# Kernel optimization log

Hardware: AMD Instinct MI355X
Metric: run time of the kernel (lower is better)

## Reference

```python
import jax, jax.numpy as jnp
import numpy as np

B, IN = 8192, 8000
C, S, O = 16, 500, 64          # num_chunks, chunk_size, fc_repr_dim
F = C * O                       # fc_0_out_feat = 1024
E, D, T = 8, 512, 2            # num_experts, fc_task_dim, num_tasks
NC = (32, 2)                    # num_classes per task
EPS = 1e-5


def _bn(h, g, b, axis):
    # training-mode BatchNorm1d: biased variance over the batch axis
    m = h.mean(axis=axis, keepdims=True)
    v = h.var(axis=axis, keepdims=True)
    return (h - m) * jax.lax.rsqrt(v + EPS) * g + b


def _swish(x):
    return x * jax.nn.sigmoid(x)


def setup_inputs() -> dict:
    key = jax.random.key(0)
    ks = jax.random.split(key, 10)
    s = 0.02
    return {
        "x": jax.random.normal(ks[0], (B, IN), dtype=jnp.float32),
        "w0": jax.random.normal(ks[1], (C, O, S), dtype=jnp.float32) * s,
        "b0": jnp.zeros((F,), jnp.float32),
        "bn0_g": jnp.ones((F,), jnp.float32),
        "bn0_b": jnp.zeros((F,), jnp.float32),
        "gate_w": jax.random.normal(ks[2], (T, F, E), dtype=jnp.float32) * s,
        "gate_b": jnp.zeros((T, E), jnp.float32),
        "exp_w": jax.random.normal(ks[3], (E, F, D), dtype=jnp.float32) * s,
        "exp_bn_g": jnp.ones((E, D), jnp.float32),
        "exp_bn_b": jnp.zeros((E, D), jnp.float32),
        "task_w": jax.random.normal(ks[4], (T, D, D), dtype=jnp.float32) * s,
        "task_bn_g": jnp.ones((T, D), jnp.float32),
        "task_bn_b": jnp.zeros((T, D), jnp.float32),
        "fin_w_a": jax.random.normal(ks[5], (D, NC[0]), dtype=jnp.float32) * s,
        "fin_b_a": jnp.zeros((NC[0],), jnp.float32),
        "fin_w_b": jax.random.normal(ks[6], (D, NC[1]), dtype=jnp.float32) * s,
        "fin_b_b": jnp.zeros((NC[1],), jnp.float32),
    }


def reference(x, w0, b0, bn0_g, bn0_b, gate_w, gate_b, exp_w, exp_bn_g,
              exp_bn_b, task_w, task_bn_g, task_bn_b, fin_w_a, fin_b_a,
              fin_w_b, fin_b_b):
    b = x.shape[0]
    # SplitLinear: block-diagonal linear over C chunks of size S -> O each
    h0 = jnp.einsum('bcs,cos->bco', x.reshape(b, C, S), w0).reshape(b, F) + b0
    h0 = _swish(_bn(h0, bn0_g, bn0_b, axis=0))                  # [B, F]
    # per-task gates with softmax over experts
    gates = jax.nn.softmax(
        jnp.einsum('bf,tfe->tbe', h0, gate_w) + gate_b[:, None, :], axis=-1)
    # expert branches: Linear(no bias) + BN + Swish, vectorized over experts
    eh = jnp.einsum('bf,efd->bed', h0, exp_w)                   # [B, E, D]
    eh = _swish(_bn(eh, exp_bn_g, exp_bn_b, axis=0))
    # gate-weighted sum over experts, per task
    mix = jnp.einsum('tbe,bed->tbd', gates, eh)                 # [T, B, D]
    # task branches: Linear(no bias) + BN + Swish
    th = jnp.einsum('tbd,tdk->tbk', mix, task_w)
    th = _swish(_bn(th, task_bn_g[:, None, :], task_bn_b[:, None, :], axis=1))
    out_a = th[0] @ fin_w_a + fin_b_a                           # [B, 32]
    out_b = th[1] @ fin_w_b + fin_b_b                           # [B, 2]
    return jnp.concatenate([out_a, out_b], axis=1)             # [B, 34]
```

## Files before the change

kernel.cpp:

```cpp
#include <hip/hip_runtime.h>
#include <math.h>

#define B_ 8192
#define IN_ 8000
#define C_ 16
#define S_ 500
#define O_ 64
#define F_ 1024
#define E_ 8
#define D_ 512
#define T_ 2
#define OUTW 34
#define EPS_ 1e-5f

typedef __attribute__((ext_vector_type(8))) short bf16x8;
typedef __attribute__((ext_vector_type(4))) float f32x4;

__device__ __forceinline__ float swishf(float x) {
    return x / (1.0f + __expf(-x));
}

__device__ __forceinline__ unsigned short f2bf(float f) {
    union { float f; unsigned u; } c;
    c.f = f;
    unsigned r = c.u + 0x7fffu + ((c.u >> 16) & 1u);
    return (unsigned short)(r >> 16);
}
__device__ __forceinline__ float bf2f(unsigned short b) {
    union { unsigned u; float f; } c;
    c.u = ((unsigned)b) << 16;
    return c.f;
}

__device__ __forceinline__ void gld16(const void* g, void* l) {
    __builtin_amdgcn_global_load_lds(
        (const __attribute__((address_space(1))) void*)g,
        (__attribute__((address_space(3))) void*)l, 16, 0, 0);
}

__global__ __launch_bounds__(256) void k_split(const float* __restrict__ x,
                                               const float* __restrict__ w0,
                                               const float* __restrict__ b0,
                                               unsigned short* __restrict__ h0raw,
                                               float* __restrict__ psum,
                                               float* __restrict__ psq) {
    __shared__ __align__(16) unsigned short As[128 * 72];
    __shared__ __align__(16) unsigned short Bs[64 * 72];
    int tid = threadIdx.x;
    int c = blockIdx.y;
    int brow0 = blockIdx.x * 128;
    const float* xp = x + (size_t)brow0 * IN_ + c * S_;
    const float* wp = w0 + (size_t)c * O_ * S_;

    int w = tid >> 6, lane = tid & 63;
    int l15 = lane & 15, quad = lane >> 4;
    int wm = w * 32;

    f32x4 acc[2][4] = {};

    for (int k0 = 0; k0 < 512; k0 += 64) {
#pragma unroll
        for (int i = 0; i < 8; i++) {
            int li = tid + i * 256;
            int row = li >> 4, c4 = li & 15;
            int gk = k0 + c4 * 4;
            float4 v = make_float4(0.f, 0.f, 0.f, 0.f);
            if (gk + 3 < S_) v = *(const float4*)(xp + (size_t)row * IN_ + gk);
            unsigned short u[4] = { f2bf(v.x), f2bf(v.y), f2bf(v.z), f2bf(v.w) };
            *(ushort4*)&As[row * 72 + c4 * 4] = *(ushort4*)u;
        }
#pragma unroll
        for (int i = 0; i < 4; i++) {
            int li = tid + i * 256;
            int row = li >> 4, c4 = li & 15;
            int gk = k0 + c4 * 4;
            float4 v = make_float4(0.f, 0.f, 0.f, 0.f);
            if (gk + 3 < S_) v = *(const float4*)(wp + (size_t)row * S_ + gk);
            unsigned short u[4] = { f2bf(v.x), f2bf(v.y), f2bf(v.z), f2bf(v.w) };
            *(ushort4*)&Bs[row * 72 + c4 * 4] = *(ushort4*)u;
        }
        __syncthreads();
#pragma unroll
        for (int kk = 0; kk < 64; kk += 32) {
            bf16x8 af[2], wf[4];
#pragma unroll
            for (int i = 0; i < 2; i++)
                af[i] = *(const bf16x8*)&As[(wm + i * 16 + l15) * 72 + kk + quad * 8];
#pragma unroll
            for (int j = 0; j < 4; j++)
                wf[j] = *(const bf16x8*)&Bs[(j * 16 + l15) * 72 + kk + quad * 8];
#pragma unroll
            for (int i = 0; i < 2; i++)
#pragma unroll
                for (int j = 0; j < 4; j++)
                    acc[i][j] = __builtin_amdgcn_mfma_f32_16x16x32_bf16(af[i], wf[j], acc[i][j], 0, 0, 0);
        }
        __syncthreads();
    }

    int colbase = c * O_;
    float sj[4], qj[4];
#pragma unroll
    for (int j = 0; j < 4; j++) {
        int col = j * 16 + l15;
        float bb = b0[colbase + col];
        float s = 0.f, q = 0.f;
#pragma unroll
        for (int i = 0; i < 2; i++) {
#pragma unroll
            for (int reg = 0; reg < 4; reg++) {
                float v = acc[i][j][reg] + bb;
                int rl = wm + i * 16 + quad * 4 + reg;
                h0raw[(size_t)(brow0 + rl) * F_ + colbase + col] = f2bf(v);
                s += v; q += v * v;
            }
        }
        s += __shfl_down(s, 32, 64); s += __shfl_down(s, 16, 64);
        q += __shfl_down(q, 32, 64); q += __shfl_down(q, 16, 64);
        sj[j] = s; qj[j] = q;
    }
    __syncthreads();
    float* red = (float*)As;
    if (lane < 16) {
#pragma unroll
        for (int j = 0; j < 4; j++) {
            int col = j * 16 + l15;
            red[col * 4 + w] = sj[j];
            red[256 + col * 4 + w] = qj[j];
        }
    }
    __syncthreads();
    if (tid < 64) {
        float ss = red[tid * 4] + red[tid * 4 + 1] + red[tid * 4 + 2] + red[tid * 4 + 3];
        float qq = red[256 + tid * 4] + red[256 + tid * 4 + 1] + red[256 + tid * 4 + 2] + red[256 + tid * 4 + 3];
        size_t idx = (size_t)blockIdx.x * F_ + colbase + tid;
        psum[idx] = ss; psq[idx] = qq;
    }
}

__global__ __launch_bounds__(64) void k_stats_b(const float* __restrict__ psum,
                                                const float* __restrict__ psq,
                                                int N, int YS,
                                                const float* __restrict__ g,
                                                const float* __restrict__ beta,
                                                unsigned long long gslab,
                                                float* __restrict__ scale,
                                                float* __restrict__ shift,
                                                unsigned long long oslab) {
    int n = blockIdx.x * 64 + threadIdx.x;
    int z = blockIdx.z;
    float s = 0.f, q = 0.f;
    for (int y = 0; y < YS; y++) {
        size_t idx = ((size_t)(z * YS + y)) * N + n;
        s += psum[idx]; q += psq[idx];
    }
    float mean = s * (1.0f / B_);
    float var = q * (1.0f / B_) - mean * mean;
    float sc = g[z * gslab + n] * rsqrtf(var + EPS_);
    scale[z * oslab + n] = sc;
    shift[z * oslab + n] = beta[z * gslab + n] - mean * sc;
}

__global__ __launch_bounds__(256) void k_wt(const float* __restrict__ in,
                                            unsigned short* __restrict__ out,
                                            int K, int N) {
    __shared__ float t[32][33];
    int k0 = blockIdx.x * 32, n0 = blockIdx.y * 32, z = blockIdx.z;
    const float* ip = in + (size_t)z * K * N;
    unsigned short* op = out + (size_t)z * N * K;
    int tn = threadIdx.x & 31, tk = threadIdx.x >> 5;
#pragma unroll
    for (int p = 0; p < 4; p++) {
        int k = tk + p * 8;
        t[k][tn] = ip[(size_t)(k0 + k) * N + n0 + tn];
    }
    __syncthreads();
    int tk2 = threadIdx.x & 31, tn2 = threadIdx.x >> 5;
#pragma unroll
    for (int p = 0; p < 4; p++) {
        int n = tn2 + p * 8;
        op[(size_t)(n0 + n) * K + k0 + tk2] = f2bf(t[tk2][n]);
    }
}

__global__ __launch_bounds__(256) void k_bnswish(const unsigned short* __restrict__ h0,
                                                 const float* __restrict__ scale,
                                                 const float* __restrict__ shift,
                                                 unsigned short* __restrict__ h0bf) {
    int tid = threadIdx.x;
    int f0 = tid * 4;
    float4 sc4 = *(const float4*)(scale + f0);
    float4 sh4 = *(const float4*)(shift + f0);
    float scv[4] = { sc4.x, sc4.y, sc4.z, sc4.w };
    float shv[4] = { sh4.x, sh4.y, sh4.z, sh4.w };
    size_t base = (size_t)blockIdx.x * 4 * F_ + f0;
#pragma unroll
    for (int r = 0; r < 4; r++) {
        ushort4 u = *(const ushort4*)(h0 + base + (size_t)r * F_);
        unsigned short uu[4] = { u.x, u.y, u.z, u.w };
        unsigned short ov[4];
#pragma unroll
        for (int j = 0; j < 4; j++)
            ov[j] = f2bf(swishf(scv[j] * bf2f(uu[j]) + shv[j]));
        *(ushort4*)(h0bf + base + (size_t)r * F_) = *(ushort4*)ov;
    }
}

__global__ __launch_bounds__(256) void k_gates(const unsigned short* __restrict__ h0bf,
                                               const float* __restrict__ gate_w,
                                               const float* __restrict__ gate_b,
                                               float* __restrict__ gates) {
    __shared__ __align__(16) unsigned short gwt[16 * 1032];
    int tid = threadIdx.x;
    for (int idx = tid; idx < 16 * 1024; idx += 256) {
        int col = idx >> 10, f = idx & 1023;
        int t = col >> 3, e = col & 7;
        gwt[col * 1032 + f] = f2bf(gate_w[(size_t)t * (F_ * E_) + (size_t)f * E_ + e]);
    }
    __syncthreads();
    int w = tid >> 6, lane = tid & 63;
    int l15 = lane & 15, quad = lane >> 4;
    int r0 = blockIdx.x * 128 + w * 32;
    f32x4 acc[2] = {};
    const unsigned short* a0p = h0bf + (size_t)(r0 + l15) * F_ + quad * 8;
    const unsigned short* a1p = a0p + (size_t)16 * F_;
    const unsigned short* wp = &gwt[l15 * 1032 + quad * 8];
#pragma unroll 4
    for (int k0 = 0; k0 < F_; k0 += 32) {
        bf16x8 wf  = *(const bf16x8*)(wp + k0);
        bf16x8 af0 = *(const bf16x8*)(a0p + k0);
        bf16x8 af1 = *(const bf16x8*)(a1p + k0);
        acc[0] = __builtin_amdgcn_mfma_f32_16x16x32_bf16(af0, wf, acc[0], 0, 0, 0);
        acc[1] = __builtin_amdgcn_mfma_f32_16x16x32_bf16(af1, wf, acc[1], 0, 0, 0);
    }
    float gb = gate_b[l15];
    int t = l15 >> 3, e = l15 & 7;
#pragma unroll
    for (int i = 0; i < 2; i++) {
#pragma unroll
        for (int reg = 0; reg < 4; reg++) {
            float v = acc[i][reg] + gb;
            float m = v;
            m = fmaxf(m, __shfl_xor(m, 1, 64));
            m = fmaxf(m, __shfl_xor(m, 2, 64));
            m = fmaxf(m, __shfl_xor(m, 4, 64));
            float ex = __expf(v - m);
            float s = ex;
            s += __shfl_xor(s, 1, 64);
            s += __shfl_xor(s, 2, 64);
            s += __shfl_xor(s, 4, 64);
            int row = r0 + i * 16 + quad * 4 + reg;
            gates[(size_t)t * (B_ * E_) + (size_t)row * E_ + e] = ex / s;
        }
    }
}

__global__ __launch_bounds__(256) void k_gemm_bf16(const unsigned short* __restrict__ A,
                                                   unsigned long long aslab,
                                                   const unsigned short* __restrict__ Wt,
                                                   unsigned long long wslab,
                                                   unsigned short* __restrict__ C,
                                                   unsigned long long cslab, int K,
                                                   float* __restrict__ psum,
                                                   float* __restrict__ psq) {
    __shared__ __align__(16) unsigned short As[128 * 32];
    __shared__ __align__(16) unsigned short Ws[128 * 32];
    int z = blockIdx.z;
    A  += (size_t)z * aslab;
    Wt += (size_t)z * wslab;
    C  += (size_t)z * cslab;
    const int N = gridDim.y * 128;
    int row0 = blockIdx.x * 128, col0 = blockIdx.y * 128;
    int tid = threadIdx.x;
    int w = tid >> 6, lane = tid & 63;
    int l15 = lane & 15, quad = lane >> 4;

    const unsigned short* ga0 = A  + (size_t)(row0 + w * 32 + (lane >> 2)) * K + (lane & 3) * 8;
    const unsigned short* ga1 = ga0 + 16 * (size_t)K;
    const unsigned short* gw0 = Wt + (size_t)(col0 + w * 32 + (lane >> 2)) * K + (lane & 3) * 8;
    const unsigned short* gw1 = gw0 + 16 * (size_t)K;
    unsigned short* la0 = As + (w * 32) * 32;
    unsigned short* la1 = As + (w * 32 + 16) * 32;
    unsigned short* lw0 = Ws + (w * 32) * 32;
    unsigned short* lw1 = Ws + (w * 32 + 16) * 32;

    int wm = (w & 1) * 64, wn = (w >> 1) * 64;
    const unsigned short* Afr = As + (size_t)(wm + l15) * 32 + quad * 8;
    const unsigned short* Wfr = Ws + (size_t)(wn + l15) * 32 + quad * 8;

    f32x4 acc[4][4] = {};

    for (int k0 = 0; k0 < K; k0 += 32) {
        gld16(ga0 + k0, la0);
        gld16(ga1 + k0, la1);
        gld16(gw0 + k0, lw0);
        gld16(gw1 + k0, lw1);
        __syncthreads();
        bf16x8 af[4], wf[4];
#pragma unroll
        for (int i = 0; i < 4; i++) af[i] = *(const bf16x8*)(Afr + i * 16 * 32);
#pragma unroll
        for (int j = 0; j < 4; j++) wf[j] = *(const bf16x8*)(Wfr + j * 16 * 32);
#pragma unroll
        for (int i = 0; i < 4; i++)
#pragma unroll
            for (int j = 0; j < 4; j++)
                acc[i][j] = __builtin_amdgcn_mfma_f32_16x16x32_bf16(af[i], wf[j], acc[i][j], 0, 0, 0);
        __syncthreads();
    }

#pragma unroll
    for (int i = 0; i < 4; i++) {
        int r = row0 + wm + i * 16 + quad * 4;
#pragma unroll
        for (int j = 0; j < 4; j++) {
            int cc = col0 + wn + j * 16 + l15;
            unsigned short* cp = C + (size_t)r * N + cc;
#pragma unroll
            for (int reg = 0; reg < 4; reg++)
                cp[(size_t)reg * N] = f2bf(acc[i][j][reg]);
        }
    }

    float* red = (float*)As;
    float sj[4], qj[4];
#pragma unroll
    for (int j = 0; j < 4; j++) {
        float s = 0.f, q = 0.f;
#pragma unroll
        for (int i = 0; i < 4; i++)
#pragma unroll
            for (int reg = 0; reg < 4; reg++) {
                float v = acc[i][j][reg];
                s += v; q += v * v;
            }
        s += __shfl_down(s, 32, 64); s += __shfl_down(s, 16, 64);
        q += __shfl_down(q, 32, 64); q += __shfl_down(q, 16, 64);
        sj[j] = s; qj[j] = q;
    }
    if (lane < 16) {
#pragma unroll
        for (int j = 0; j < 4; j++) {
            int cib = wn + j * 16 + lane;
            red[cib * 2 + (w & 1)] = sj[j];
            red[256 + cib * 2 + (w & 1)] = qj[j];
        }
    }
    __syncthreads();
    if (tid < 128) {
        float s = red[tid * 2] + red[tid * 2 + 1];
        float q = red[256 + tid * 2] + red[256 + tid * 2 + 1];
        size_t row = (size_t)z * gridDim.x + blockIdx.x;
        psum[row * N + col0 + tid] = s;
        psq[row * N + col0 + tid] = q;
    }
}

__global__ __launch_bounds__(512, 2) void k_gemm256(const unsigned short* __restrict__ A,
                                                    const unsigned short* __restrict__ Wt,
                                                    unsigned short* __restrict__ Cc,
                                                    int N, int K,
                                                    float* __restrict__ psum,
                                                    float* __restrict__ psq) {
    __shared__ __align__(16) unsigned short lds[2][2][2][8192];
    int tid = threadIdx.x;
    int w = tid >> 6, lane = tid & 63;
    int l15 = lane & 15, quad = lane >> 4;
    int wm = w >> 2, wn = w & 3;

    int lin = blockIdx.y * gridDim.x + blockIdx.x;
    int cpx = (gridDim.x * gridDim.y) >> 3;
    int swz = (lin & 7) * cpx + (lin >> 3);
    int bx = swz & (gridDim.x - 1), by = swz / gridDim.x;
    int row0 = bx * 256, col0 = by * 256;

    int srow = tid >> 3, sperm = (tid & 7) ^ (srow & 7);
    const unsigned short* pA = A  + (size_t)(row0 + srow) * K + sperm * 8;
    const unsigned short* pB = Wt + (size_t)(col0 + srow) * K + sperm * 8;

    int aoffs[2];
#pragma unroll
    for (int kk = 0; kk < 2; kk++)
        aoffs[kk] = l15 * 64 + ((kk * 4 + quad) ^ (l15 & 7)) * 8;

    f32x4 acc[8][4] = {};
    bf16x8 afr[4][2], bfr[2][2];
    int nt = K >> 6;

#define STAGE256(t1, nb) do {                                                              \
    const unsigned short* sA = pA + (size_t)(t1) * 64;                                     \
    const unsigned short* sB = pB + (size_t)(t1) * 64;                                     \
    _Pragma("unroll")                                                                      \
    for (int h = 0; h < 2; h++)                                                            \
        _Pragma("unroll")                                                                  \
        for (int L = 0; L < 2; L++) {                                                      \
            gld16(sA + (size_t)(h * 128 + L * 64) * K, &lds[nb][0][h][w * 512 + L * 4096]);\
            gld16(sB + (size_t)(h * 128 + L * 64) * K, &lds[nb][1][h][w * 512 + L * 4096]);\
        }                                                                                  \
} while (0)

#define LDA256(mh) do {                                                                    \
    _Pragma("unroll")                                                                      \
    for (int mf = 0; mf < 4; mf++)                                                         \
        _Pragma("unroll")                                                                  \
        for (int kk = 0; kk < 2; kk++)                                                     \
            afr[mf][kk] = *(const bf16x8*)(Ab + ((mh) * 4 + mf) * 1024 + aoffs[kk]);       \
} while (0)

#define LDB256(nh) do {                                                                    \
    _Pragma("unroll")                                                                      \
    for (int nf = 0; nf < 2; nf++)                                                         \
        _Pragma("unroll")                                                                  \
        for (int kk = 0; kk < 2; kk++)                                                     \
            bfr[nf][kk] = *(const bf16x8*)(Bb + ((nh) * 2 + nf) * 1024 + aoffs[kk]);       \
} while (0)

#define MMA256(mh, nh) do {                                                                \
    _Pragma("unroll")                                                                      \
    for (int mf = 0; mf < 4; mf++)                                                         \
        _Pragma("unroll")                                                                  \
        for (int nf = 0; nf < 2; nf++)                                                     \
            _Pragma("unroll")                                                              \
            for (int kk = 0; kk < 2; kk++)                                                 \
                acc[(mh) * 4 + mf][(nh) * 2 + nf] = __builtin_amdgcn_mfma_f32_16x16x32_bf16(\
                    afr[mf][kk], bfr[nf][kk], acc[(mh) * 4 + mf][(nh) * 2 + nf], 0, 0, 0); \
} while (0)

#define PHASE_MID()                                                                        \
    __builtin_amdgcn_s_barrier();                                                          \
    asm volatile("s_waitcnt lgkmcnt(0)" ::: "memory");                                     \
    __builtin_amdgcn_sched_barrier(0);                                                     \
    __builtin_amdgcn_s_setprio(1);

#define PHASE_END()                                                                        \
    __builtin_amdgcn_s_setprio(0);                                                         \
    __builtin_amdgcn_sched_barrier(0);                                                     \
    __builtin_amdgcn_s_barrier();

    STAGE256(0, 0);
    asm volatile("s_waitcnt vmcnt(0)" ::: "memory");
    __builtin_amdgcn_s_barrier();

    for (int t = 0; t < nt; t++) {
        int buf = t & 1;
        const unsigned short* Ab = &lds[buf][0][wm][0];
        const unsigned short* Bb = &lds[buf][1][wn >> 1][(wn & 1) * 4096];
        LDA256(0); LDB256(0);
        if (t + 1 < nt) STAGE256(t + 1, buf ^ 1);
        PHASE_MID();
        MMA256(0, 0);
        PHASE_END();
        LDB256(1);
        PHASE_MID();
        MMA256(0, 1);
        PHASE_END();
        LDA256(1);
        PHASE_MID();
        MMA256(1, 1);
        PHASE_END();
        LDB256(0);
        PHASE_MID();
        MMA256(1, 0);
        __builtin_amdgcn_s_setprio(0);
        __builtin_amdgcn_sched_barrier(0);
        asm volatile("s_waitcnt vmcnt(0)" ::: "memory");
        __builtin_amdgcn_s_barrier();
    }
#undef STAGE256
#undef LDA256
#undef LDB256
#undef MMA256
#undef PHASE_MID
#undef PHASE_END

    __syncthreads();

#pragma unroll
    for (int mf = 0; mf < 8; mf++) {
        int r = row0 + wm * 128 + mf * 16 + quad * 4;
#pragma unroll
        for (int nf = 0; nf < 4; nf++) {
            int cc = col0 + wn * 64 + nf * 16 + l15;
            unsigned short* cp = Cc + (size_t)r * N + cc;
#pragma unroll
            for (int reg = 0; reg < 4; reg++)
                cp[(size_t)reg * N] = f2bf(acc[mf][nf][reg]);
        }
    }

    float* red = (float*)&lds[0][0][0][0];
    float* redq = red + 512;
    float sj[4], qj[4];
#pragma unroll
    for (int nf = 0; nf < 4; nf++) {
        float s = 0.f, q = 0.f;
#pragma unroll
        for (int mf = 0; mf < 8; mf++)
#pragma unroll
            for (int reg = 0; reg < 4; reg++) {
                float v = acc[mf][nf][reg];
                s += v; q += v * v;
            }
        s += __shfl_down(s, 32, 64); s += __shfl_down(s, 16, 64);
        q += __shfl_down(q, 32, 64); q += __shfl_down(q, 16, 64);
        sj[nf] = s; qj[nf] = q;
    }
    if (quad == 0) {
#pragma unroll
        for (int nf = 0; nf < 4; nf++) {
            int cib = wn * 64 + nf * 16 + l15;
            red[cib * 2 + wm] = sj[nf];
            redq[cib * 2 + wm] = qj[nf];
        }
    }
    __syncthreads();
    if (tid < 256) {
        float s = red[tid * 2] + red[tid * 2 + 1];
        float q = redq[tid * 2] + redq[tid * 2 + 1];
        psum[(size_t)bx * N + col0 + tid] = s;
        psq [(size_t)bx * N + col0 + tid] = q;
    }
}

__global__ __launch_bounds__(256) void k_mix(const unsigned short* __restrict__ eh,
                                             const float* __restrict__ scale,
                                             const float* __restrict__ shift,
                                             const float* __restrict__ gates,
                                             unsigned short* __restrict__ mix) {
    __shared__ float scl[E_ * D_], shl[E_ * D_];
    __shared__ float gl[2][2][8];
    int tid = threadIdx.x;
#pragma unroll
    for (int i = 0; i < 4; i++) {
        int li = tid + i * 256;
        ((float4*)scl)[li] = ((const float4*)scale)[li];
        ((float4*)shl)[li] = ((const float4*)shift)[li];
    }
    if (tid < 32) {
        int sub = tid >> 4, t = (tid >> 3) & 1, e = tid & 7;
        gl[sub][t][e] = gates[(size_t)t * (B_ * E_) + (size_t)(blockIdx.x * 2 + sub) * E_ + e];
    }
    __syncthreads();
    int sub = tid >> 7;
    int b = blockIdx.x * 2 + sub;
    int d0 = (tid & 127) * 4;
    float a0[4] = {0.f, 0.f, 0.f, 0.f}, a1[4] = {0.f, 0.f, 0.f, 0.f};
#pragma unroll
    for (int e = 0; e < E_; e++) {
        ushort4 u = *(const ushort4*)&eh[(size_t)b * (E_ * D_) + e * D_ + d0];
        float4 sc4 = *(const float4*)&scl[e * D_ + d0];
        float4 sh4 = *(const float4*)&shl[e * D_ + d0];
        float g0 = gl[sub][0][e], g1 = gl[sub][1][e];
        unsigned short uu[4] = { u.x, u.y, u.z, u.w };
        float scv[4] = { sc4.x, sc4.y, sc4.z, sc4.w };
        float shv[4] = { sh4.x, sh4.y, sh4.z, sh4.w };
#pragma unroll
        for (int l = 0; l < 4; l++) {
            float sw = swishf(scv[l] * bf2f(uu[l]) + shv[l]);
            a0[l] += g0 * sw;
            a1[l] += g1 * sw;
        }
    }
    unsigned short o0[4], o1[4];
#pragma unroll
    for (int l = 0; l < 4; l++) { o0[l] = f2bf(a0[l]); o1[l] = f2bf(a1[l]); }
    *(ushort4*)&mix[(size_t)b * D_ + d0] = *(ushort4*)o0;
    *(ushort4*)&mix[(size_t)(B_ * D_) + (size_t)b * D_ + d0] = *(ushort4*)o1;
}

__global__ __launch_bounds__(256) void k_final(const unsigned short* __restrict__ th,
                                               const float* __restrict__ scale,
                                               const float* __restrict__ shift,
                                               const float* __restrict__ fwa,
                                               const float* __restrict__ fba,
                                               const float* __restrict__ fwb,
                                               const float* __restrict__ fbb,
                                               float* __restrict__ out) {
    __shared__ float t0[8][D_], t1[8][D_];
    __shared__ float pb[64];
    int tid = threadIdx.x;
    int b0 = blockIdx.x * 8;
#pragma unroll
    for (int t = 0; t < 2; t++) {
#pragma unroll
        for (int i = 0; i < 4; i++) {
            int li = tid + i * 256;
            int row = li >> 7, d = (li & 127) * 4;
            ushort4 u = *(const ushort4*)&th[((size_t)t * B_ + b0 + row) * D_ + d];
            unsigned short uu[4] = { u.x, u.y, u.z, u.w };
            float* dst = t ? &t1[row][d] : &t0[row][d];
#pragma unroll
            for (int l = 0; l < 4; l++)
                dst[l] = swishf(scale[t * D_ + d + l] * bf2f(uu[l]) + shift[t * D_ + d + l]);
        }
    }
    __syncthreads();
    {
        int row = tid >> 5, col = tid & 31;
        float a0 = 0.f, a1 = 0.f, a2 = 0.f, a3 = 0.f;
        for (int d = 0; d < D_; d += 4) {
            a0 += t0[row][d + 0] * fwa[(d + 0) * 32 + col];
            a1 += t0[row][d + 1] * fwa[(d + 1) * 32 + col];
            a2 += t0[row][d + 2] * fwa[(d + 2) * 32 + col];
            a3 += t0[row][d + 3] * fwa[(d + 3) * 32 + col];
        }
        out[(size_t)(b0 + row) * OUTW + col] = fba[col] + ((a0 + a1) + (a2 + a3));
    }
    if (tid < 64) {
        int row = tid >> 3, colb = (tid >> 2) & 1, part = tid & 3;
        float a = 0.f;
        for (int d = part * 128; d < part * 128 + 128; d += 2) {
            a += t1[row][d] * fwb[d * 2 + colb];
            a += t1[row][d + 1] * fwb[(d + 1) * 2 + colb];
        }
        pb[tid] = a;
    }
    __syncthreads();
    if (tid < 16) {
        int row = tid >> 1, colb = tid & 1;
        int base = row * 8 + colb * 4;
        float a = fbb[colb] + pb[base] + pb[base + 1] + pb[base + 2] + pb[base + 3];
        out[(size_t)(b0 + row) * OUTW + 32 + colb] = a;
    }
}

extern "C" void kernel_launch(void* const* d_in, const int* in_sizes, int n_in,
                              void* d_out, int out_size, void* d_ws, size_t ws_size,
                              hipStream_t stream) {
    const float* x        = (const float*)d_in[0];
    const float* w0       = (const float*)d_in[1];
    const float* b0       = (const float*)d_in[2];
    const float* bn0_g    = (const float*)d_in[3];
    const float* bn0_b    = (const float*)d_in[4];
    const float* gate_w   = (const float*)d_in[5];
    const float* gate_b   = (const float*)d_in[6];
    const float* exp_w    = (const float*)d_in[7];
    const float* exp_bn_g = (const float*)d_in[8];
    const float* exp_bn_b = (const float*)d_in[9];
    const float* task_w   = (const float*)d_in[10];
    const float* task_bn_g= (const float*)d_in[11];
    const float* task_bn_b= (const float*)d_in[12];
    const float* fwa      = (const float*)d_in[13];
    const float* fba      = (const float*)d_in[14];
    const float* fwb      = (const float*)d_in[15];
    const float* fbb      = (const float*)d_in[16];
    float* out = (float*)d_out;

    float* ws = (float*)d_ws;
    unsigned short* ehbf  = (unsigned short*)ws;
    unsigned short* h0raw = (unsigned short*)(ws + 16777216);
    unsigned short* thbf  = ehbf;
    unsigned short* mixbf = h0raw;
    unsigned short* h0bf  = (unsigned short*)(ws + 20971520);
    unsigned short* wtE   = (unsigned short*)(ws + 25165824);
    unsigned short* twt   = (unsigned short*)(ws + 27262976);
    float* gates = ws + 27525120;
    float* sc0   = ws + 27656192;
    float* sh0   = sc0 + 1024;
    float* scE   = sh0 + 1024;
    float* shE   = scE + 4096;
    float* scT   = shE + 4096;
    float* shT   = scT + 1024;
    float* psum  = shT + 1024;
    float* psq   = psum + 262144;

    k_wt<<<dim3(32, 16, 8), 256, 0, stream>>>(exp_w, wtE, F_, D_);
    k_wt<<<dim3(16, 16, 2), 256, 0, stream>>>(task_w, twt, D_, D_);
    k_split<<<dim3(64, 16), 256, 0, stream>>>(x, w0, b0, h0raw, psum, psq);
    k_stats_b<<<dim3(16, 1, 1), 64, 0, stream>>>(psum, psq, F_, 64, bn0_g, bn0_b, 0ull, sc0, sh0, 0ull);
    k_bnswish<<<dim3(B_ / 4), 256, 0, stream>>>(h0raw, sc0, sh0, h0bf);
    k_gates<<<dim3(B_ / 128), 256, 0, stream>>>(h0bf, gate_w, gate_b, gates);
    k_gemm256<<<dim3(32, 16), 512, 0, stream>>>(h0bf, wtE, ehbf, E_ * D_, F_, psum, psq);
    k_stats_b<<<dim3(64, 1, 1), 64, 0, stream>>>(psum, psq, E_ * D_, 32, exp_bn_g, exp_bn_b, 0ull, scE, shE, 0ull);
    k_mix<<<dim3(B_ / 2), 256, 0, stream>>>(ehbf, scE, shE, gates, mixbf);
    k_gemm_bf16<<<dim3(64, 4, 2), 256, 0, stream>>>(mixbf, (unsigned long long)(B_ * D_),
                                                    twt, (unsigned long long)(D_ * D_),
                                                    thbf, (unsigned long long)(B_ * D_), D_,
                                                    psum, psq);
    k_stats_b<<<dim3(8, 1, 2), 64, 0, stream>>>(psum, psq, D_, 64, task_bn_g, task_bn_b, 512ull, scT, shT, 512ull);
    k_final<<<dim3(B_ / 8), 256, 0, stream>>>(thbf, scT, shT, fwa, fba, fwb, fbb, out);
}
```

Measured before the change: 648.2 us.

## Software-pipeline global loads in split-linear and bf16 GEMM kernels

In the split-linear kernel, the next K-tile of x and w0 is prefetched into registers while the MFMAs for the current tile run, and is written to shared memory at the start of the next iteration. In the bf16 GEMM, shared memory is double-buffered so the async global-to-LDS copy for tile t+1 is issued before computing tile t, dropping one barrier per iteration. The aim is to hide global memory latency behind compute. The cost is more registers in k_split and twice the LDS in the GEMM, which may lower occupancy. The GEMM also relies on the single barrier at the end of each iteration for correctness of the async copies.

```diff
diff --git a/kernel.cpp b/kernel.cpp
--- a/kernel.cpp
+++ b/kernel.cpp
@@ -56,30 +56,46 @@
     int l15 = lane & 15, quad = lane >> 4;
     int wm = w * 32;
 
+    int srow = tid >> 4, sc4 = tid & 15;
+    int gkbase = sc4 * 4;
+
     f32x4 acc[2][4] = {};
-
-    for (int k0 = 0; k0 < 512; k0 += 64) {
-#pragma unroll
-        for (int i = 0; i < 8; i++) {
-            int li = tid + i * 256;
-            int row = li >> 4, c4 = li & 15;
-            int gk = k0 + c4 * 4;
-            float4 v = make_float4(0.f, 0.f, 0.f, 0.f);
-            if (gk + 3 < S_) v = *(const float4*)(xp + (size_t)row * IN_ + gk);
-            unsigned short u[4] = { f2bf(v.x), f2bf(v.y), f2bf(v.z), f2bf(v.w) };
-            *(ushort4*)&As[row * 72 + c4 * 4] = *(ushort4*)u;
-        }
-#pragma unroll
-        for (int i = 0; i < 4; i++) {
-            int li = tid + i * 256;
-            int row = li >> 4, c4 = li & 15;
-            int gk = k0 + c4 * 4;
-            float4 v = make_float4(0.f, 0.f, 0.f, 0.f);
-            if (gk + 3 < S_) v = *(const float4*)(wp + (size_t)row * S_ + gk);
-            unsigned short u[4] = { f2bf(v.x), f2bf(v.y), f2bf(v.z), f2bf(v.w) };
-            *(ushort4*)&Bs[row * 72 + c4 * 4] = *(ushort4*)u;
-        }
+    float4 ra[8], rw[4];
+
+#define LOAD_AB(k0) do {                                                                   \
+    int gk = (k0) + gkbase;                                                                \
+    bool ok = (gk + 3 < S_);                                                               \
+    _Pragma("unroll")                                                                      \
+    for (int i = 0; i < 8; i++) {                                                          \
+        ra[i] = make_float4(0.f, 0.f, 0.f, 0.f);                                           \
+        if (ok) ra[i] = *(const float4*)(xp + (size_t)(srow + i * 16) * IN_ + gk);         \
+    }                                                                                      \
+    _Pragma("unroll")                                                                      \
+    for (int i = 0; i < 4; i++) {                                                          \
+        rw[i] = make_float4(0.f, 0.f, 0.f, 0.f);                                           \
+        if (ok) rw[i] = *(const float4*)(wp + (size_t)(srow + i * 16) * S_ + gk);          \
+    }                                                                                      \
+} while (0)
+
+#define WRITE_AB() do {                                                                    \
+    _Pragma("unroll")                                                                      \
+    for (int i = 0; i < 8; i++) {                                                          \
+        unsigned short u[4] = { f2bf(ra[i].x), f2bf(ra[i].y), f2bf(ra[i].z), f2bf(ra[i].w) };\
+        *(ushort4*)&As[(srow + i * 16) * 72 + sc4 * 4] = *(ushort4*)u;                     \
+    }                                                                                      \
+    _Pragma("unroll")                                                                      \
+    for (int i = 0; i < 4; i++) {                                                          \
+        unsigned short u[4] = { f2bf(rw[i].x), f2bf(rw[i].y), f2bf(rw[i].z), f2bf(rw[i].w) };\
+        *(ushort4*)&Bs[(srow + i * 16) * 72 + sc4 * 4] = *(ushort4*)u;                     \
+    }                                                                                      \
+} while (0)
+
+    LOAD_AB(0);
+#pragma unroll
+    for (int it = 0; it < 8; it++) {
+        WRITE_AB();
         __syncthreads();
+        if (it < 7) LOAD_AB((it + 1) * 64);
 #pragma unroll
         for (int kk = 0; kk < 64; kk += 32) {
             bf16x8 af[2], wf[4];
@@ -97,6 +113,8 @@
         }
         __syncthreads();
     }
+#undef LOAD_AB
+#undef WRITE_AB
 
     int colbase = c * O_;
     float sj[4], qj[4];
@@ -263,8 +281,8 @@
                                                    unsigned long long cslab, int K,
                                                    float* __restrict__ psum,
                                                    float* __restrict__ psq) {
-    __shared__ __align__(16) unsigned short As[128 * 32];
-    __shared__ __align__(16) unsigned short Ws[128 * 32];
+    __shared__ __align__(16) unsigned short As[2][128 * 32];
+    __shared__ __align__(16) unsigned short Ws[2][128 * 32];
     int z = blockIdx.z;
     A  += (size_t)z * aslab;
     Wt += (size_t)z * wslab;
@@ -279,23 +297,29 @@
     const unsigned short* ga1 = ga0 + 16 * (size_t)K;
     const unsigned short* gw0 = Wt + (size_t)(col0 + w * 32 + (lane >> 2)) * K + (lane & 3) * 8;
     const unsigned short* gw1 = gw0 + 16 * (size_t)K;
-    unsigned short* la0 = As + (w * 32) * 32;
-    unsigned short* la1 = As + (w * 32 + 16) * 32;
-    unsigned short* lw0 = Ws + (w * 32) * 32;
-    unsigned short* lw1 = Ws + (w * 32 + 16) * 32;
+    int lo_a = (w * 32) * 32;
+    int lo_w = (w * 32) * 32;
 
     int wm = (w & 1) * 64, wn = (w >> 1) * 64;
-    const unsigned short* Afr = As + (size_t)(wm + l15) * 32 + quad * 8;
-    const unsigned short* Wfr = Ws + (size_t)(wn + l15) * 32 + quad * 8;
 
     f32x4 acc[4][4] = {};
 
-    for (int k0 = 0; k0 < K; k0 += 32) {
-        gld16(ga0 + k0, la0);
-        gld16(ga1 + k0, la1);
-        gld16(gw0 + k0, lw0);
-        gld16(gw1 + k0, lw1);
-        __syncthreads();
+#define STAGE_T(k0, b) do {                                   \
+    gld16(ga0 + (k0), &As[b][lo_a]);                          \
+    gld16(ga1 + (k0), &As[b][lo_a + 16 * 32]);                \
+    gld16(gw0 + (k0), &Ws[b][lo_w]);                          \
+    gld16(gw1 + (k0), &Ws[b][lo_w + 16 * 32]);                \
+} while (0)
+
+    STAGE_T(0, 0);
+    __syncthreads();
+
+    int nk = K >> 5;
+    for (int t = 0; t < nk; t++) {
+        int cur = t & 1;
+        if (t + 1 < nk) STAGE_T((t + 1) * 32, cur ^ 1);
+        const unsigned short* Afr = &As[cur][(wm + l15) * 32 + quad * 8];
+        const unsigned short* Wfr = &Ws[cur][(wn + l15) * 32 + quad * 8];
         bf16x8 af[4], wf[4];
 #pragma unroll
         for (int i = 0; i < 4; i++) af[i] = *(const bf16x8*)(Afr + i * 16 * 32);
@@ -308,6 +332,7 @@
                 acc[i][j] = __builtin_amdgcn_mfma_f32_16x16x32_bf16(af[i], wf[j], acc[i][j], 0, 0, 0);
         __syncthreads();
     }
+#undef STAGE_T
 
 #pragma unroll
     for (int i = 0; i < 4; i++) {
@@ -322,7 +347,7 @@
         }
     }
 
-    float* red = (float*)As;
+    float* red = (float*)&As[0][0];
     float sj[4], qj[4];
 #pragma unroll
     for (int j = 0; j < 4; j++) {
```

Measured after the change: 654.4 us. Within noise of the previous version (+1.0%).
